# Optimization experiments

Hardware: AMD Instinct MI355X
Metric: run time of the kernel (lower is better)

The kernel has to match this reference:

```python
import jax, jax.numpy as jnp
import numpy as np

HIDDEN = 1024
HEADS = 16
HEAD_DIM = HIDDEN // HEADS


def setup_inputs() -> dict:
    key = jax.random.key(0)
    kx, kw = jax.random.split(key)
    x = jax.random.normal(kx, (1, 4096, HIDDEN), dtype=jnp.float32)
    # torch Linear weight is [out, in]; we store as [in, out] for x @ W
    W_qkv = jax.random.normal(kw, (HIDDEN, 3 * HIDDEN), dtype=jnp.float32) * (HIDDEN ** -0.5)
    return {"x": x, "W_qkv": W_qkv}


def reference(x, W_qkv):
    B, T, _ = x.shape
    qkv = x @ W_qkv                                    # [B, T, 3*HIDDEN]
    qkv = qkv.reshape(B, T, 3, HEADS, HEAD_DIM)
    qkv = jnp.transpose(qkv, (2, 0, 3, 1, 4))          # [3, B, H, T, Dh]
    q, k, v = qkv[0], qkv[1], qkv[2]
    scale = HEAD_DIM ** -0.5
    attn = jnp.einsum("bhqd,bhkd->bhqk", q, k) * scale  # [B, H, T, T] materialized (naive)
    attn = jax.nn.softmax(attn, axis=-1)
    out = jnp.einsum("bhqk,bhkd->bhqd", attn, v)        # [B, H, T, Dh]
    out = jnp.transpose(out, (0, 2, 1, 3)).reshape(B, T, HIDDEN)
    return out
```

## Files before the change

kernel.cpp:

```cpp
#include <hip/hip_runtime.h>

#define SEQ 4096
#define HID 1024
#define NH  16
#define DH  64
#define N3  3072

typedef __attribute__((ext_vector_type(4))) float floatx4;
typedef __attribute__((ext_vector_type(8))) short shortx8;
typedef __attribute__((ext_vector_type(4))) short shortx4;

__device__ __forceinline__ short f2bf(float f) {
    return (short)((__builtin_bit_cast(unsigned, f) + 0x8000u) >> 16);
}
__device__ __forceinline__ unsigned pk2bf(float a, float b) {
    unsigned ua = __builtin_bit_cast(unsigned, a) + 0x8000u;
    unsigned ub = __builtin_bit_cast(unsigned, b) + 0x8000u;
    return (ua >> 16) | (ub & 0xFFFF0000u);
}
__device__ __forceinline__ shortx4 pk4bf(float a, float b, float c, float d) {
    union { unsigned u[2]; shortx4 s; } x;
    x.u[0] = pk2bf(a, b);
    x.u[1] = pk2bf(c, d);
    return x.s;
}

#if __has_builtin(__builtin_amdgcn_exp2f)
#define fexp2 __builtin_amdgcn_exp2f
#else
#define fexp2 exp2f
#endif

#define mfma32 __builtin_amdgcn_mfma_f32_16x16x32_bf16

__device__ __forceinline__ void gll16(const short* g, short* l) {
    __builtin_amdgcn_global_load_lds(
        (const __attribute__((address_space(1))) unsigned*)g,
        (__attribute__((address_space(3))) unsigned*)l, 16, 0, 0);
}

__global__ __launch_bounds__(256) void convert_x(
    const float* __restrict__ x, short* __restrict__ Xb)
{
    size_t i = (size_t)blockIdx.x * 256 + threadIdx.x;
    float4 v = *(const float4*)&x[i * 4];
    shortx4 b = pk4bf(v.x, v.y, v.z, v.w);
    *(shortx4*)&Xb[i * 4] = b;
}

__global__ __launch_bounds__(256) void transpose_W(
    const float* __restrict__ W, short* __restrict__ Wt)
{
    __shared__ short Ws[128 * 40];
    const int t  = threadIdx.x;
    const int n0 = blockIdx.x * 128;
    const int k0 = blockIdx.y * 32;
    #pragma unroll
    for (int i = 0; i < 4; i++) {
        int idx = t + i * 256;
        int k = idx >> 5, c4 = idx & 31;
        float4 v = *(const float4*)&W[(size_t)(k0 + k) * N3 + n0 + c4 * 4];
        Ws[(c4 * 4 + 0) * 40 + k] = f2bf(v.x);
        Ws[(c4 * 4 + 1) * 40 + k] = f2bf(v.y);
        Ws[(c4 * 4 + 2) * 40 + k] = f2bf(v.z);
        Ws[(c4 * 4 + 3) * 40 + k] = f2bf(v.w);
    }
    __syncthreads();
    #pragma unroll
    for (int i = 0; i < 2; i++) {
        int idx = t + i * 256;
        int n = idx >> 2, seg = idx & 3;
        shortx8 g = *(const shortx8*)&Ws[n * 40 + seg * 8];
        *(shortx8*)&Wt[(size_t)(n0 + n) * HID + k0 + seg * 8] = g;
    }
}

#define LDC 136
__global__ __launch_bounds__(256) void qkv_gemm(
    const short* __restrict__ Xb, const short* __restrict__ Wt,
    short* __restrict__ Qb, short* __restrict__ Kb, short* __restrict__ Vb)
{
    __shared__ short SM[18432];
    short* As = SM;
    short* Bs = SM + 128 * 64;
    const int tid  = threadIdx.x;
    const int m0   = blockIdx.x * 128;
    const int n0   = blockIdx.y * 128;
    const int lane = tid & 63;
    const int wid  = tid >> 6;
    const int wm   = (wid >> 1) * 64;
    const int wn   = (wid & 1) * 64;
    const int l15  = lane & 15;
    const int quad = lane >> 4;

    floatx4 acc[4][4];
    #pragma unroll
    for (int i = 0; i < 4; i++)
        #pragma unroll
        for (int j = 0; j < 4; j++)
            acc[i][j] = (floatx4){0.f, 0.f, 0.f, 0.f};

    const int arow = tid >> 3, ac = tid & 7;
    const int swk  = (ac ^ (arow & 7)) << 3;
    const short* ag = Xb + (size_t)(m0 + arow) * HID + swk;
    const short* bg = Wt + (size_t)(n0 + arow) * HID + swk;
    short* al = As + (size_t)(tid & 192) * 8;
    short* bl = Bs + (size_t)(tid & 192) * 8;
    const int r7 = l15 & 7;

    for (int k0 = 0; k0 < HID; k0 += 64) {
        #pragma unroll
        for (int i = 0; i < 4; i++)
            gll16(ag + (size_t)i * 32 * HID + k0, al + i * 2048);
        #pragma unroll
        for (int i = 0; i < 4; i++)
            gll16(bg + (size_t)i * 32 * HID + k0, bl + i * 2048);
        __syncthreads();
        #pragma unroll
        for (int kh = 0; kh < 2; kh++) {
            shortx8 af[4], bf[4];
            #pragma unroll
            for (int t = 0; t < 4; t++) {
                int R = wm + t * 16 + l15;
                af[t] = *(const shortx8*)&As[(R << 6) + ((((kh << 2) + quad) ^ r7) << 3)];
                int Rb = wn + t * 16 + l15;
                bf[t] = *(const shortx8*)&Bs[(Rb << 6) + ((((kh << 2) + quad) ^ r7) << 3)];
            }
            #pragma unroll
            for (int tm = 0; tm < 4; tm++)
                #pragma unroll
                for (int tn = 0; tn < 4; tn++)
                    acc[tm][tn] = mfma32(af[tm], bf[tn], acc[tm][tn], 0, 0, 0);
        }
        __syncthreads();
    }

    short* Cs = SM;
    const float sc = (n0 < 1024) ? 0.18033688011112042f : 1.0f;
    #pragma unroll
    for (int tm = 0; tm < 4; tm++)
        #pragma unroll
        for (int tn = 0; tn < 4; tn++)
            #pragma unroll
            for (int r = 0; r < 4; r++)
                Cs[(wm + tm * 16 + quad * 4 + r) * LDC + wn + tn * 16 + l15] =
                    f2bf(acc[tm][tn][r] * sc);
    __syncthreads();
    short* base = (n0 < 1024) ? Qb : (n0 < 2048 ? Kb : Vb);
    const int h0 = (n0 & 1023) >> 6;
    #pragma unroll
    for (int j = 0; j < 8; j++) {
        int idx = tid + j * 256;
        int row = idx >> 4, col = (idx & 15) * 8;
        shortx8 v = *(const shortx8*)&Cs[row * LDC + col];
        *(shortx8*)&base[((size_t)(h0 + (col >> 6)) * SEQ + m0 + row) * DH + (col & 63)] = v;
    }
}

__global__ __launch_bounds__(256) void transpose_V(
    const short* __restrict__ Vb, short* __restrict__ Vt)
{
    __shared__ short Ts[64 * 72];
    const int t  = threadIdx.x;
    const int t0 = blockIdx.x * 64;
    const int h  = blockIdx.y;
    #pragma unroll
    for (int i = 0; i < 2; i++) {
        int idx = t + i * 256;
        int r = idx >> 3, seg = idx & 7;
        shortx8 g = *(const shortx8*)&Vb[((size_t)h * SEQ + t0 + r) * DH + seg * 8];
        *(shortx8*)&Ts[r * 72 + seg * 8] = g;
    }
    __syncthreads();
    #pragma unroll
    for (int i = 0; i < 2; i++) {
        int idx = t + i * 256;
        int d = idx >> 3, tseg = idx & 7;
        shortx8 g;
        #pragma unroll
        for (int j = 0; j < 8; j++) g[j] = Ts[(tseg * 8 + j) * 72 + d];
        *(shortx8*)&Vt[((size_t)h * DH + d) * SEQ + t0 + tseg * 8] = g;
    }
}

__global__ __launch_bounds__(256) void flash_attn(
    const short* __restrict__ Qb, const short* __restrict__ Kb,
    const short* __restrict__ Vt, float* __restrict__ out,
    float* __restrict__ Opart, float* __restrict__ Lpart,
    int kpc, int nit, int final)
{
    __shared__ short Ks[2][4096];
    __shared__ short Vs[2][4096];
    const int tid  = threadIdx.x;
    const int lane = tid & 63;
    const int l15  = lane & 15;
    const int quad = lane >> 4;
    const int h    = blockIdx.y;
    const int ch   = blockIdx.z;
    const int q0   = blockIdx.x * 128 + (tid >> 6) * 32;
    const int tstart = ch * kpc;
    const shortx8 ones8 = {(short)0x3F80, (short)0x3F80, (short)0x3F80, (short)0x3F80,
                           (short)0x3F80, (short)0x3F80, (short)0x3F80, (short)0x3F80};

    const short* qp = Qb + ((size_t)h * SEQ + q0 + l15) * DH;
    shortx8 qf00 = *(const shortx8*)(qp + quad * 8);
    shortx8 qf01 = *(const shortx8*)(qp + 32 + quad * 8);
    shortx8 qf10 = *(const shortx8*)(qp + 16 * DH + quad * 8);
    shortx8 qf11 = *(const shortx8*)(qp + 16 * DH + 32 + quad * 8);

    floatx4 oacc[2][4];
    #pragma unroll
    for (int s = 0; s < 2; s++)
        #pragma unroll
        for (int dn = 0; dn < 4; dn++)
            oacc[s][dn] = (floatx4){0.f, 0.f, 0.f, 0.f};
    floatx4 lacc0 = {0.f, 0.f, 0.f, 0.f}, lacc1 = {0.f, 0.f, 0.f, 0.f};

    const int rK   = tid >> 3, sK = tid & 7;
    const int key0 = 8 * ((rK >> 2) & 3) + 4 * ((rK >> 4) & 1) + (rK & 3);
    const int swo  = (sK ^ (rK & 7)) << 3;
    const short* kg = Kb + ((size_t)h * SEQ + tstart + key0) * DH + swo;
    const short* vg = Vt + ((size_t)h * DH + rK) * SEQ + tstart + swo;
    const int wslot = (tid & 192) * 8;

    gll16(kg,            &Ks[0][wslot]);
    gll16(kg + 32 * DH,  &Ks[0][wslot + 2048]);
    gll16(vg,            &Vs[0][wslot]);
    gll16(vg + 32 * SEQ, &Vs[0][wslot + 2048]);
    kg += 64 * DH;  vg += 64;

    for (int it = 0; it < nit; it++) {
        __syncthreads();
        if (it + 1 < nit) {
            int b = (it + 1) & 1;
            gll16(kg,            &Ks[b][wslot]);
            gll16(kg + 32 * DH,  &Ks[b][wslot + 2048]);
            gll16(vg,            &Vs[b][wslot]);
            gll16(vg + 32 * SEQ, &Vs[b][wslot + 2048]);
            kg += 64 * DH;  vg += 64;
        }
        const short* ks = Ks[it & 1];
        const short* vs = Vs[it & 1];

        floatx4 st0[4], st1[4];
        #pragma unroll
        for (int tn = 0; tn < 4; tn++) {
            int R = tn * 16 + l15;
            int off = (R << 6) + ((quad ^ (R & 7)) << 3);
            shortx8 kf0 = *(const shortx8*)&ks[off];
            shortx8 kf1 = *(const shortx8*)&ks[off ^ 32];
            floatx4 a0 = {0.f, 0.f, 0.f, 0.f};
            a0 = mfma32(kf0, qf00, a0, 0, 0, 0);
            a0 = mfma32(kf1, qf01, a0, 0, 0, 0);
            st0[tn] = a0;
            floatx4 a1 = {0.f, 0.f, 0.f, 0.f};
            a1 = mfma32(kf0, qf10, a1, 0, 0, 0);
            a1 = mfma32(kf1, qf11, a1, 0, 0, 0);
            st1[tn] = a1;
        }

        union { unsigned u[4]; shortx8 s; } pa00, pa01, pa10, pa11;
        #pragma unroll
        for (int half = 0; half < 2; half++) {
            int ta = half * 2, tb = half * 2 + 1;
            unsigned* d0 = half ? pa01.u : pa00.u;
            unsigned* d1 = half ? pa11.u : pa10.u;
            d0[0] = pk2bf(fexp2(st0[ta][0]), fexp2(st0[ta][1]));
            d0[1] = pk2bf(fexp2(st0[ta][2]), fexp2(st0[ta][3]));
            d0[2] = pk2bf(fexp2(st0[tb][0]), fexp2(st0[tb][1]));
            d0[3] = pk2bf(fexp2(st0[tb][2]), fexp2(st0[tb][3]));
            d1[0] = pk2bf(fexp2(st1[ta][0]), fexp2(st1[ta][1]));
            d1[1] = pk2bf(fexp2(st1[ta][2]), fexp2(st1[ta][3]));
            d1[2] = pk2bf(fexp2(st1[tb][0]), fexp2(st1[tb][1]));
            d1[3] = pk2bf(fexp2(st1[tb][2]), fexp2(st1[tb][3]));
        }

        lacc0 = mfma32(pa00.s, ones8, lacc0, 0, 0, 0);
        lacc0 = mfma32(pa01.s, ones8, lacc0, 0, 0, 0);
        lacc1 = mfma32(pa10.s, ones8, lacc1, 0, 0, 0);
        lacc1 = mfma32(pa11.s, ones8, lacc1, 0, 0, 0);

        #pragma unroll
        for (int dn = 0; dn < 4; dn++) {
            int row = dn * 16 + l15;
            int off = (row << 6) + ((quad ^ (row & 7)) << 3);
            shortx8 va = *(const shortx8*)&vs[off];
            shortx8 vb = *(const shortx8*)&vs[off ^ 32];
            oacc[0][dn] = mfma32(pa00.s, va, oacc[0][dn], 0, 0, 0);
            oacc[0][dn] = mfma32(pa01.s, vb, oacc[0][dn], 0, 0, 0);
            oacc[1][dn] = mfma32(pa10.s, va, oacc[1][dn], 0, 0, 0);
            oacc[1][dn] = mfma32(pa11.s, vb, oacc[1][dn], 0, 0, 0);
        }
    }

    if (final) {
        #pragma unroll
        for (int r = 0; r < 4; r++) {
            float rl0 = 1.0f / lacc0[r], rl1 = 1.0f / lacc1[r];
            int query = q0 + quad * 4 + r;
            float* d0 = out + (size_t)query * HID + h * DH + l15;
            float* d1 = d0 + (size_t)16 * HID;
            #pragma unroll
            for (int dn = 0; dn < 4; dn++) {
                d0[dn * 16] = oacc[0][dn][r] * rl0;
                d1[dn * 16] = oacc[1][dn][r] * rl1;
            }
        }
    } else {
        #pragma unroll
        for (int r = 0; r < 4; r++) {
            int query = q0 + quad * 4 + r;
            float* d0 = Opart + ((size_t)ch * SEQ + query) * HID + h * DH + l15;
            float* d1 = d0 + (size_t)16 * HID;
            #pragma unroll
            for (int dn = 0; dn < 4; dn++) {
                d0[dn * 16] = oacc[0][dn][r];
                d1[dn * 16] = oacc[1][dn][r];
            }
        }
        if (l15 == 0) {
            float* lp = Lpart + ((size_t)ch * NH + h) * SEQ + q0;
            #pragma unroll
            for (int r = 0; r < 4; r++) {
                lp[quad * 4 + r]      = lacc0[r];
                lp[16 + quad * 4 + r] = lacc1[r];
            }
        }
    }
}

__global__ __launch_bounds__(256) void combine(
    const float* __restrict__ Opart, const float* __restrict__ Lpart,
    float* __restrict__ out, int chn)
{
    size_t i = ((size_t)blockIdx.x * 256 + threadIdx.x) * 4;
    int q = (int)(i >> 10);
    int h = ((int)i & 1023) >> 6;
    float4 o = {0.f, 0.f, 0.f, 0.f};
    float l = 0.f;
    for (int c = 0; c < chn; c++) {
        float4 p = *(const float4*)&Opart[(size_t)c * SEQ * HID + i];
        o.x += p.x; o.y += p.y; o.z += p.z; o.w += p.w;
        l += Lpart[((size_t)c * NH + h) * SEQ + q];
    }
    float rl = 1.0f / l;
    float4 r = {o.x * rl, o.y * rl, o.z * rl, o.w * rl};
    *(float4*)&out[i] = r;
}

extern "C" void kernel_launch(void* const* d_in, const int* in_sizes, int n_in,
                              void* d_out, int out_size, void* d_ws, size_t ws_size,
                              hipStream_t stream) {
    const float* x = (const float*)d_in[0];
    const float* W = (const float*)d_in[1];
    float* out = (float*)d_out;

    short* Xb = (short*)d_ws;
    short* Wt = Xb + (size_t)SEQ * HID;
    short* Qb = Wt + (size_t)N3 * HID;
    short* Kb = Qb + (size_t)NH * SEQ * DH;
    short* Vb = Kb + (size_t)NH * SEQ * DH;
    short* Vt = Xb;
    float* Opart = (float*)(Vb + (size_t)NH * SEQ * DH);

    const size_t need = 39845888ull
                      + 4ull * SEQ * HID * 4
                      + 4ull * NH * SEQ * 4;
    const int chn = (ws_size >= need) ? 4 : 1;
    float* Lpart = Opart + (size_t)chn * SEQ * HID;
    const int kpc = SEQ / chn, nit = kpc / 64;

    convert_x  <<<dim3(SEQ * HID / 1024), 256, 0, stream>>>(x, Xb);
    transpose_W<<<dim3(N3 / 128, HID / 32), 256, 0, stream>>>(W, Wt);
    qkv_gemm   <<<dim3(SEQ / 128, N3 / 128), 256, 0, stream>>>(Xb, Wt, Qb, Kb, Vb);
    transpose_V<<<dim3(SEQ / 64, NH), 256, 0, stream>>>(Vb, Vt);
    flash_attn <<<dim3(SEQ / 128, NH, chn), 256, 0, stream>>>(
        Qb, Kb, Vt, out, Opart, Lpart, kpc, nit, chn == 1);
    if (chn > 1)
        combine<<<dim3(SEQ * HID / 1024), 256, 0, stream>>>(Opart, Lpart, out, chn);
}
```

Before: 215.3 us.

## Remap attention blocks across XCDs, add setprio, hardware bf16 pack, fewer KV chunks

The attention kernel now remaps its linear block index so consecutive work items are spread across the eight XCDs. It raises wave priority around the MFMA sections with s_setprio and replaces the software bf16 rounding with the v_cvt_pk_bf16_f32 instruction. The host cuts the key-split count from 4 to 2, which halves the partial-output traffic and combine work but also halves the grid size. The remap hardcodes the grid shape, assuming 32 query blocks and 16 heads.

```diff
diff --git a/kernel.cpp b/kernel.cpp
--- a/kernel.cpp
+++ b/kernel.cpp
@@ -23,6 +23,12 @@
     x.u[0] = pk2bf(a, b);
     x.u[1] = pk2bf(c, d);
     return x.s;
+}
+
+__device__ __forceinline__ unsigned cvtpk(float lo, float hi) {
+    unsigned r;
+    asm("v_cvt_pk_bf16_f32 %0, %1, %2" : "=v"(r) : "v"(lo), "v"(hi));
+    return r;
 }
 
 #if __has_builtin(__builtin_amdgcn_exp2f)
@@ -195,9 +201,13 @@
     const int lane = tid & 63;
     const int l15  = lane & 15;
     const int quad = lane >> 4;
-    const int h    = blockIdx.y;
-    const int ch   = blockIdx.z;
-    const int q0   = blockIdx.x * 128 + (tid >> 6) * 32;
+
+    const int nblk = (int)(gridDim.x * gridDim.y * gridDim.z);
+    const int lin  = (int)blockIdx.x + ((int)blockIdx.y << 5) + ((int)blockIdx.z << 9);
+    const int work = (lin & 7) * (nblk >> 3) + (lin >> 3);
+    const int h    = (work >> 5) & 15;
+    const int ch   = work >> 9;
+    const int q0   = (work & 31) * 128 + (tid >> 6) * 32;
     const int tstart = ch * kpc;
     const shortx8 ones8 = {(short)0x3F80, (short)0x3F80, (short)0x3F80, (short)0x3F80,
                            (short)0x3F80, (short)0x3F80, (short)0x3F80, (short)0x3F80};
@@ -243,6 +253,7 @@
         const short* vs = Vs[it & 1];
 
         floatx4 st0[4], st1[4];
+        __builtin_amdgcn_s_setprio(1);
         #pragma unroll
         for (int tn = 0; tn < 4; tn++) {
             int R = tn * 16 + l15;
@@ -258,6 +269,7 @@
             a1 = mfma32(kf1, qf11, a1, 0, 0, 0);
             st1[tn] = a1;
         }
+        __builtin_amdgcn_s_setprio(0);
 
         union { unsigned u[4]; shortx8 s; } pa00, pa01, pa10, pa11;
         #pragma unroll
@@ -265,16 +277,17 @@
             int ta = half * 2, tb = half * 2 + 1;
             unsigned* d0 = half ? pa01.u : pa00.u;
             unsigned* d1 = half ? pa11.u : pa10.u;
-            d0[0] = pk2bf(fexp2(st0[ta][0]), fexp2(st0[ta][1]));
-            d0[1] = pk2bf(fexp2(st0[ta][2]), fexp2(st0[ta][3]));
-            d0[2] = pk2bf(fexp2(st0[tb][0]), fexp2(st0[tb][1]));
-            d0[3] = pk2bf(fexp2(st0[tb][2]), fexp2(st0[tb][3]));
-            d1[0] = pk2bf(fexp2(st1[ta][0]), fexp2(st1[ta][1]));
-            d1[1] = pk2bf(fexp2(st1[ta][2]), fexp2(st1[ta][3]));
-            d1[2] = pk2bf(fexp2(st1[tb][0]), fexp2(st1[tb][1]));
-            d1[3] = pk2bf(fexp2(st1[tb][2]), fexp2(st1[tb][3]));
-        }
-
+            d0[0] = cvtpk(fexp2(st0[ta][0]), fexp2(st0[ta][1]));
+            d0[1] = cvtpk(fexp2(st0[ta][2]), fexp2(st0[ta][3]));
+            d0[2] = cvtpk(fexp2(st0[tb][0]), fexp2(st0[tb][1]));
+            d0[3] = cvtpk(fexp2(st0[tb][2]), fexp2(st0[tb][3]));
+            d1[0] = cvtpk(fexp2(st1[ta][0]), fexp2(st1[ta][1]));
+            d1[1] = cvtpk(fexp2(st1[ta][2]), fexp2(st1[ta][3]));
+            d1[2] = cvtpk(fexp2(st1[tb][0]), fexp2(st1[tb][1]));
+            d1[3] = cvtpk(fexp2(st1[tb][2]), fexp2(st1[tb][3]));
+        }
+
+        __builtin_amdgcn_s_setprio(1);
         lacc0 = mfma32(pa00.s, ones8, lacc0, 0, 0, 0);
         lacc0 = mfma32(pa01.s, ones8, lacc0, 0, 0, 0);
         lacc1 = mfma32(pa10.s, ones8, lacc1, 0, 0, 0);
@@ -291,6 +304,7 @@
             oacc[1][dn] = mfma32(pa10.s, va, oacc[1][dn], 0, 0, 0);
             oacc[1][dn] = mfma32(pa11.s, vb, oacc[1][dn], 0, 0, 0);
         }
+        __builtin_amdgcn_s_setprio(0);
     }
 
     if (final) {
@@ -364,9 +378,9 @@
     float* Opart = (float*)(Vb + (size_t)NH * SEQ * DH);
 
     const size_t need = 39845888ull
-                      + 4ull * SEQ * HID * 4
-                      + 4ull * NH * SEQ * 4;
-    const int chn = (ws_size >= need) ? 4 : 1;
+                      + 2ull * SEQ * HID * 4
+                      + 2ull * NH * SEQ * 4;
+    const int chn = (ws_size >= need) ? 2 : 1;
     float* Lpart = Opart + (size_t)chn * SEQ * HID;
     const int kpc = SEQ / chn, nit = kpc / 64;
 
```

After: 201.6 us. -6.4%, faster.
